# Optimization experiments

Hardware: AMD Instinct MI355X
Metric: run time of the kernel (lower is better)

The kernel has to match this reference:

```python
import jax, jax.numpy as jnp
import numpy as np

R = 4
D = 2 * R + 1  # 9
B, C, H, W = 1, 256, 48, 96


def setup_inputs() -> dict:
    key = jax.random.key(0)
    k1, k2, k3, k4, k5 = jax.random.split(key, 5)
    f1 = jax.random.normal(k1, (B, C, H, W), dtype=jnp.float32)
    f2 = jax.random.normal(k2, (B, C, H, W), dtype=jnp.float32)
    cx = jax.random.uniform(k3, (B, H, W), dtype=jnp.float32) * (W - 1)
    cy = jax.random.uniform(k4, (B, H, W), dtype=jnp.float32) * (H - 1)
    coords = jnp.stack([cx, cy], axis=1)  # (B,2,H,W), ch0=x, ch1=y
    # DAP: 1x1 conv over (2r+1)^2 channels, identity init (perturbed so it is non-trivial)
    w_dap = jnp.eye(D * D, dtype=jnp.float32) + 0.02 * jax.random.normal(k5, (D * D, D * D), dtype=jnp.float32)
    return {"f1": f1, "f2": f2, "coords": coords, "w_dap": w_dap}


def _bilinear_sample(img, px, py):
    # img: (C,H,W); px,py: (M,) pixel coords; zeros padding, align_corners=True semantics
    c, h, w = img.shape
    x0 = jnp.floor(px)
    y0 = jnp.floor(py)
    x1 = x0 + 1.0
    y1 = y0 + 1.0
    wx1 = px - x0
    wx0 = 1.0 - wx1
    wy1 = py - y0
    wy0 = 1.0 - wy1
    flat = img.reshape(c, h * w)

    def corner(xi, yi, wgt):
        valid = (xi >= 0) & (xi <= w - 1) & (yi >= 0) & (yi <= h - 1)
        xc = jnp.clip(xi, 0, w - 1).astype(jnp.int32)
        yc = jnp.clip(yi, 0, h - 1).astype(jnp.int32)
        v = flat[:, yc * w + xc]  # (C,M)
        return v * (wgt * valid.astype(wgt.dtype))[None, :]

    return (corner(x0, y0, wx0 * wy0) + corner(x1, y0, wx1 * wy0)
            + corner(x0, y1, wx0 * wy1) + corner(x1, y1, wx1 * wy1))


def _corr_forward(f1, f2, coords, w_dap):
    b, c, h, w = f1.shape
    d = jnp.linspace(-R, R, D, dtype=f1.dtype)
    # centroids[b, i, y, j, x] = (coords_x + dx[i], coords_y + dy[j])
    px = coords[:, 0][:, None, :, None, :] + d[None, :, None, None, None]  # (B,D,H,1,W)->(B,D,H,D,W)
    py = coords[:, 1][:, None, :, None, :] + d[None, None, None, :, None]
    px = jnp.broadcast_to(px, (b, D, h, D, w)).reshape(b, -1)
    py = jnp.broadcast_to(py, (b, D, h, D, w)).reshape(b, -1)
    samp = jax.vmap(_bilinear_sample)(f2, px, py)  # (B, C, D*H*D*W)
    f2s = samp.reshape(b, c, D, h, D, w)
    corr = jnp.einsum('bcihjw,bchw->bijhw', f2s, f1) / jnp.sqrt(jnp.asarray(c, f1.dtype))
    cf = corr.reshape(b, D * D, h, w)
    out = jnp.einsum('od,bdhw->bohw', w_dap, cf)  # DAP 1x1 conv, no bias
    return out  # (B, (2r+1)^2, H, W)


def reference(f1, f2, coords, w_dap):
    return _corr_forward(f1, f2, coords, w_dap)
```

## Files before the change

### kernel.cpp

```cpp
#include <hip/hip_runtime.h>

#define HH   48
#define WW   96
#define CC   256
#define RRAD 4
#define DD   9
#define DD2  81
#define PP   10
#define HWSZ (HH * WW)
#define ROWB 512
#define ZOFF ((unsigned)HWSZ * ROWB)

typedef __attribute__((ext_vector_type(8))) short short8v;
typedef __attribute__((ext_vector_type(4))) float f32x4;

__device__ __forceinline__ unsigned bf16rne(float f) {
  unsigned u = __float_as_uint(f);
  return (u + 0x7FFFu + ((u >> 16) & 1u)) >> 16;
}

__device__ __forceinline__ void gload_lds16(const char* g, char* l) {
  __builtin_amdgcn_global_load_lds(
      (const __attribute__((address_space(1))) char*)g,
      (__attribute__((address_space(3))) char*)l, 16, 0, 0);
}

__global__ __launch_bounds__(256) void transpose_to_bf16(
    const float* __restrict__ f1, const float* __restrict__ f2,
    const float* __restrict__ w_dap, char* __restrict__ f2tb,
    char* __restrict__ f1tb, char* __restrict__ zpage,
    unsigned short* __restrict__ Wf) {
  __shared__ float tile[64][65];
  const float* src = (blockIdx.y == 0) ? f1 : f2;
  char* dst = (blockIdx.y == 0) ? f1tb : f2tb;

  const int tid = threadIdx.x;
  if (blockIdx.y == 0 && blockIdx.x == 0 && tid < 32) {
    float4 z = {0.f, 0.f, 0.f, 0.f};
    *(float4*)(zpage + tid * 16) = z;
  }
  if (blockIdx.y == 0 && blockIdx.x < 36) {
    int gid = blockIdx.x * 256 + tid;
    int g = gid >> 9;
    int idx = gid & 511;
    int ln = idx >> 3, e = idx & 7;
    int m = g / 3, kt = g - m * 3;
    int r = m * 16 + (ln & 15);
    int c = kt * 32 + (ln >> 4) * 8 + e;
    float v = (r < DD2 && c < DD2) ? w_dap[r * DD2 + c] : 0.f;
    Wf[gid] = (unsigned short)bf16rne(v);
  }

  const int tiles_p = HWSZ / 64;
  const int bc = blockIdx.x / tiles_p;
  const int bp = blockIdx.x % tiles_p;
  const int c0 = bc * 64, p0 = bp * 64;

#pragma unroll
  for (int k = 0; k < 16; k++) {
    int idx = k * 256 + tid;
    int cl = idx >> 6, pl = idx & 63;
    tile[cl][pl] = src[(size_t)(c0 + cl) * HWSZ + p0 + pl];
  }
  __syncthreads();
#pragma unroll
  for (int k = 0; k < 8; k++) {
    int idx = k * 256 + tid;
    int pl = idx >> 5, cp = idx & 31;
    unsigned lo = bf16rne(tile[2 * cp][pl]);
    unsigned hi = bf16rne(tile[2 * cp + 1][pl]);
    *(unsigned*)(dst + (size_t)(p0 + pl) * ROWB + (size_t)c0 * 2 + cp * 4) =
        lo | (hi << 16);
  }
}

__global__ __launch_bounds__(256, 3) void corr_main(
    const char* __restrict__ f2tb, const char* __restrict__ f1tb,
    const float* __restrict__ coords, const unsigned short* __restrict__ Wf,
    float* __restrict__ out) {
  __shared__ __align__(16) char patch[100 * ROWB];
  __shared__ unsigned rowoff[100];
  __shared__ float dots[112];
  __shared__ __align__(16) unsigned short cb[96];

  const int p = blockIdx.x;
  const int tid = threadIdx.x;

  const float cx = coords[p];
  const float cy = coords[HWSZ + p];
  const float fxf = floorf(cx), fyf = floorf(cy);
  const float fx = cx - fxf, fy = cy - fyf;
  const int xb = (int)fxf - RRAD;
  const int yb = (int)fyf - RRAD;

  if (tid < 100) {
    int yy = tid / 10, xx = tid - yy * 10;
    int gy = yb + yy, gx = xb + xx;
    rowoff[tid] = (gx >= 0 && gx < WW && gy >= 0 && gy < HH)
                      ? (unsigned)(gy * WW + gx) * ROWB : ZOFF;
  }

  const int lane = tid & 63, wid = tid >> 6;
  const int hi = lane >> 4, lo = lane & 15;

  const char* f1b = f1tb + (size_t)p * ROWB + hi * 16;
  short8v bfrag[8];
#pragma unroll
  for (int kt = 0; kt < 8; kt++) bfrag[kt] = *(const short8v*)(f1b + kt * 64);

  __syncthreads();

  {
    const int sub = lane >> 5;
    const int col = (lane & 31) * 16;
    for (int s = wid; s < 50; s += 4) {
      const int r = 2 * s + sub;
      gload_lds16(f2tb + rowoff[r] + (col ^ ((r & 7) << 4)), &patch[s * 1024]);
    }
  }
  __syncthreads();

#pragma unroll
  for (int mi = 0; mi < 2; mi++) {
    const int m = wid + mi * 4;
    if (m < 7) {
      int row = m * 16 + lo;
      row = row > 99 ? 99 : row;
      const char* rp = patch + row * ROWB;
      const int swz = (row & 7) << 4;
      short8v a[8];
#pragma unroll
      for (int kt = 0; kt < 8; kt++)
        a[kt] = *(const short8v*)(rp + ((hi * 16 + kt * 64) ^ swz));
      f32x4 acc = {0.f, 0.f, 0.f, 0.f};
#pragma unroll
      for (int kt = 0; kt < 8; kt++)
        acc = __builtin_amdgcn_mfma_f32_16x16x32_bf16(a[kt], bfrag[kt], acc, 0, 0, 0);
      if (lo == 0) {
        const int rb = m * 16 + hi * 4;
        dots[rb + 0] = acc[0];
        dots[rb + 1] = acc[1];
        dots[rb + 2] = acc[2];
        dots[rb + 3] = acc[3];
      }
    }
  }
  __syncthreads();

  if (tid < 96) {
    float c = 0.f;
    if (tid < DD2) {
      const int i = tid / DD, j = tid - i * DD;
      const float d00 = dots[j * PP + i];
      const float d01 = dots[j * PP + i + 1];
      const float d10 = dots[(j + 1) * PP + i];
      const float d11 = dots[(j + 1) * PP + i + 1];
      c = ((1.f - fy) * ((1.f - fx) * d00 + fx * d01) +
           fy * ((1.f - fx) * d10 + fx * d11)) * 0.0625f;
    }
    cb[tid] = (unsigned short)bf16rne(c);
  }
  __syncthreads();

  short8v bq[3];
#pragma unroll
  for (int kt = 0; kt < 3; kt++)
    bq[kt] = *(const short8v*)&cb[kt * 32 + hi * 8];
#pragma unroll
  for (int mi = 0; mi < 2; mi++) {
    const int m = wid + mi * 4;
    if (m < 6) {
      const unsigned short* wr = Wf + ((size_t)(m * 3) * 64 + lane) * 8;
      f32x4 acc = {0.f, 0.f, 0.f, 0.f};
#pragma unroll
      for (int kt = 0; kt < 3; kt++) {
        short8v aw = *(const short8v*)(wr + (size_t)kt * 512);
        acc = __builtin_amdgcn_mfma_f32_16x16x32_bf16(aw, bq[kt], acc, 0, 0, 0);
      }
      if (lo == 0) {
#pragma unroll
        for (int j = 0; j < 4; j++) {
          const int o = m * 16 + hi * 4 + j;
          if (o < DD2) out[(size_t)o * HWSZ + p] = acc[j];
        }
      }
    }
  }
}

extern "C" void kernel_launch(void* const* d_in, const int* in_sizes, int n_in,
                              void* d_out, int out_size, void* d_ws, size_t ws_size,
                              hipStream_t stream) {
  const float* f1     = (const float*)d_in[0];
  const float* f2     = (const float*)d_in[1];
  const float* coords = (const float*)d_in[2];
  const float* w_dap  = (const float*)d_in[3];
  float* out = (float*)d_out;

  char* f2tb  = (char*)d_ws;
  char* zpage = f2tb + (size_t)HWSZ * ROWB;
  char* f1tb  = zpage + 512;
  unsigned short* Wf = (unsigned short*)(f1tb + (size_t)HWSZ * ROWB);

  dim3 tgrid((CC / 64) * (HWSZ / 64), 2);
  transpose_to_bf16<<<tgrid, 256, 0, stream>>>(f1, f2, w_dap, f2tb, f1tb, zpage, Wf);

  corr_main<<<dim3(HWSZ), 256, 0, stream>>>(f2tb, f1tb, coords, Wf, out);
}
```

Baseline: 36.29 us.

## Replace block barriers with per-wave gather and vmcnt waits in corr_main

The separate rowoff LDS table and the two __syncthreads that guarded it are removed. Each wave now computes the gather addresses for the patch rows it will consume itself, and issues global_load_lds for them directly. f1 is also staged through LDS with global_load_lds. Each wave then waits on its own outstanding loads using tuned vmcnt counts, and does its second MFMA tile after a later wait, so the second tile's loads overlap with the first tile's compute. This relies on hand-counted vmcnt values and raw s_barrier calls, which are fragile if the compiler reorders or adds memory operations.

```diff
diff --git a/kernel.cpp b/kernel.cpp
--- a/kernel.cpp
+++ b/kernel.cpp
@@ -79,12 +79,16 @@
     const float* __restrict__ coords, const unsigned short* __restrict__ Wf,
     float* __restrict__ out) {
   __shared__ __align__(16) char patch[100 * ROWB];
-  __shared__ unsigned rowoff[100];
+  __shared__ __align__(16) char f1buf[1024];
   __shared__ float dots[112];
   __shared__ __align__(16) unsigned short cb[96];
 
   const int p = blockIdx.x;
   const int tid = threadIdx.x;
+  const int lane = tid & 63, wid = tid >> 6;
+  const int hi = lane >> 4, lo = lane & 15;
+  const int sub = lane >> 5;
+  const char* zp = f2tb + ZOFF;
 
   const float cx = coords[p];
   const float cy = coords[HWSZ + p];
@@ -93,59 +97,88 @@
   const int xb = (int)fxf - RRAD;
   const int yb = (int)fyf - RRAD;
 
-  if (tid < 100) {
-    int yy = tid / 10, xx = tid - yy * 10;
-    int gy = yb + yy, gx = xb + xx;
-    rowoff[tid] = (gx >= 0 && gx < WW && gy >= 0 && gy < HH)
-                      ? (unsigned)(gy * WW + gx) * ROWB : ZOFF;
-  }
-
-  const int lane = tid & 63, wid = tid >> 6;
-  const int hi = lane >> 4, lo = lane & 15;
-
-  const char* f1b = f1tb + (size_t)p * ROWB + hi * 16;
+  {
+    const char* fs = (lane < 32) ? (f1tb + (size_t)p * ROWB + (lane & 31) * 16)
+                                 : (zp + (lane & 31) * 16);
+    gload_lds16(fs, f1buf);
+  }
+#pragma unroll
+  for (int half = 0; half < 2; half++) {
+    const int ti = wid + half * 4;
+    if (ti < 7) {
+#pragma unroll
+      for (int rp = 0; rp < 8; rp++) {
+        const int base = ti * 16 + rp * 2;
+        if (base < 100) {
+          const int r = base + sub;
+          const int yy = (r * 205) >> 11;
+          const int xx = r - yy * 10;
+          const int gy = yb + yy, gx = xb + xx;
+          const unsigned ro = (gx >= 0 && gx < WW && gy >= 0 && gy < HH)
+                                  ? (unsigned)(gy * WW + gx) * ROWB : ZOFF;
+          const char* src =
+              f2tb + ro + (((lane & 31) * 16) ^ ((r & 7) << 4));
+          gload_lds16(src, &patch[base * ROWB]);
+        }
+      }
+    }
+  }
+
+  if (wid == 3)      asm volatile("s_waitcnt vmcnt(0)" ::: "memory");
+  else if (wid == 2) asm volatile("s_waitcnt vmcnt(2)" ::: "memory");
+  else               asm volatile("s_waitcnt vmcnt(8)" ::: "memory");
+  __builtin_amdgcn_sched_barrier(0);
+
   short8v bfrag[8];
 #pragma unroll
-  for (int kt = 0; kt < 8; kt++) bfrag[kt] = *(const short8v*)(f1b + kt * 64);
-
-  __syncthreads();
+  for (int kt = 0; kt < 8; kt++)
+    bfrag[kt] = *(const short8v*)(f1buf + hi * 16 + kt * 64);
 
   {
-    const int sub = lane >> 5;
-    const int col = (lane & 31) * 16;
-    for (int s = wid; s < 50; s += 4) {
-      const int r = 2 * s + sub;
-      gload_lds16(f2tb + rowoff[r] + (col ^ ((r & 7) << 4)), &patch[s * 1024]);
-    }
-  }
-  __syncthreads();
-
-#pragma unroll
-  for (int mi = 0; mi < 2; mi++) {
-    const int m = wid + mi * 4;
-    if (m < 7) {
-      int row = m * 16 + lo;
-      row = row > 99 ? 99 : row;
-      const char* rp = patch + row * ROWB;
-      const int swz = (row & 7) << 4;
-      short8v a[8];
-#pragma unroll
-      for (int kt = 0; kt < 8; kt++)
-        a[kt] = *(const short8v*)(rp + ((hi * 16 + kt * 64) ^ swz));
-      f32x4 acc = {0.f, 0.f, 0.f, 0.f};
-#pragma unroll
-      for (int kt = 0; kt < 8; kt++)
-        acc = __builtin_amdgcn_mfma_f32_16x16x32_bf16(a[kt], bfrag[kt], acc, 0, 0, 0);
-      if (lo == 0) {
-        const int rb = m * 16 + hi * 4;
-        dots[rb + 0] = acc[0];
-        dots[rb + 1] = acc[1];
-        dots[rb + 2] = acc[2];
-        dots[rb + 3] = acc[3];
-      }
-    }
-  }
-  __syncthreads();
+    const int m = wid;
+    int row = m * 16 + lo;
+    const char* rp2 = patch + row * ROWB;
+    const int swz = (row & 7) << 4;
+    short8v a[8];
+#pragma unroll
+    for (int kt = 0; kt < 8; kt++)
+      a[kt] = *(const short8v*)(rp2 + ((hi * 16 + kt * 64) ^ swz));
+    f32x4 acc = {0.f, 0.f, 0.f, 0.f};
+#pragma unroll
+    for (int kt = 0; kt < 8; kt++)
+      acc = __builtin_amdgcn_mfma_f32_16x16x32_bf16(a[kt], bfrag[kt], acc, 0, 0, 0);
+    if (lo == 0) {
+      const int rb = m * 16 + hi * 4;
+      dots[rb + 0] = acc[0]; dots[rb + 1] = acc[1];
+      dots[rb + 2] = acc[2]; dots[rb + 3] = acc[3];
+    }
+  }
+
+  if (wid < 3) {
+    asm volatile("s_waitcnt vmcnt(0)" ::: "memory");
+    __builtin_amdgcn_sched_barrier(0);
+    const int m = wid + 4;
+    int row = m * 16 + lo;
+    row = row > 99 ? 99 : row;
+    const char* rp2 = patch + row * ROWB;
+    const int swz = (row & 7) << 4;
+    short8v a[8];
+#pragma unroll
+    for (int kt = 0; kt < 8; kt++)
+      a[kt] = *(const short8v*)(rp2 + ((hi * 16 + kt * 64) ^ swz));
+    f32x4 acc = {0.f, 0.f, 0.f, 0.f};
+#pragma unroll
+    for (int kt = 0; kt < 8; kt++)
+      acc = __builtin_amdgcn_mfma_f32_16x16x32_bf16(a[kt], bfrag[kt], acc, 0, 0, 0);
+    if (lo == 0) {
+      const int rb = m * 16 + hi * 4;
+      dots[rb + 0] = acc[0]; dots[rb + 1] = acc[1];
+      dots[rb + 2] = acc[2]; dots[rb + 3] = acc[3];
+    }
+  }
+
+  asm volatile("s_waitcnt lgkmcnt(0)" ::: "memory");
+  __builtin_amdgcn_s_barrier();
 
   if (tid < 96) {
     float c = 0.f;
@@ -160,7 +193,8 @@
     }
     cb[tid] = (unsigned short)bf16rne(c);
   }
-  __syncthreads();
+  asm volatile("s_waitcnt lgkmcnt(0)" ::: "memory");
+  __builtin_amdgcn_s_barrier();
 
   short8v bq[3];
 #pragma unroll
```

Result: no change. 35.62 us (-1.8%).
